# Kernel optimization log

Measured on AMD Instinct MI355X. Metric: run time of the kernel, lower is better.

The kernel has to match this reference:

```python
import jax, jax.numpy as jnp
import numpy as np

FEAS = 4096  # number of sparse features
K = 64       # FM latent factor dim
B = 4096     # batch size


def setup_inputs() -> dict:
    key = jax.random.key(0)
    k1, k2, k3, k4 = jax.random.split(key, 4)
    x = jax.random.normal(k1, (B, FEAS), dtype=jnp.float32)
    # torch.rand init for the cross factor tensor (feas, 1, k)
    cross = jax.random.uniform(k2, (FEAS, 1, K), dtype=jnp.float32)
    # nn.Linear(feas, 1): weight (1, feas), bias (1,)
    bound = 1.0 / np.sqrt(FEAS)
    linear_w = jax.random.uniform(k3, (1, FEAS), dtype=jnp.float32, minval=-bound, maxval=bound)
    linear_b = jax.random.uniform(k4, (1,), dtype=jnp.float32, minval=-bound, maxval=bound)
    return {"x": x, "cross": cross, "linear_w": linear_w, "linear_b": linear_b}


def reference(x, cross, linear_w, linear_b):
    # linear part: [B, feas] @ [feas, 1] + bias -> [B, 1]
    linear = x @ linear_w.T + linear_b

    # Cross term of the original: G[i, j] = V_i . V_j (Gram matrix of factor
    # vectors), summed over the upper triangle INCLUDING the diagonal.
    # sum_{i<=j} V_i.V_j = 0.5 * (sum_{i,j} V_i.V_j + sum_i ||V_i||^2)
    #                    = 0.5 * (||sum_i V_i||^2 + sum_i ||V_i||^2)
    # This avoids materializing the (feas, feas) matrix while computing the
    # exact same scalar.
    V = cross[:, 0, :]                      # (feas, k)
    col_sum = jnp.sum(V, axis=0)            # (k,)
    total = jnp.dot(col_sum, col_sum)       # sum over all (i, j) pairs
    diag = jnp.sum(V * V)                   # sum over i == j
    cross_sum = 0.5 * (total + diag)        # scalar, triu incl. diagonal

    # Note: the cross term is input-independent in the original module
    # (it never multiplies by the input); we reproduce that faithfully.
    return jax.nn.sigmoid(linear + cross_sum)
```

## Files before the change

### kernel.cpp

```cpp
#include <hip/hip_runtime.h>
#include <math.h>

#define FEAS 4096
#define K 64
#define BATCH 4096
#define NBLK 64

typedef float floatx4 __attribute__((ext_vector_type(4)));


__global__ __launch_bounds__(256) void cross_partial_kernel(
    const float* __restrict__ cross, float* __restrict__ ws) {
    const int j  = threadIdx.x & 63;
    const int rl = threadIdx.x >> 6;
    const int row0 = blockIdx.x * 64;

    float s = 0.f, q = 0.f;
#pragma unroll
    for (int i = 0; i < 16; ++i) {
        const float v = cross[(size_t)(row0 + rl * 16 + i) * K + j];
        s += v;
        q += v * v;
    }

    __shared__ float ls[256];
    __shared__ float lq[256];
    ls[threadIdx.x] = s;
    lq[threadIdx.x] = q;
    __syncthreads();

    if (threadIdx.x < 64) {
        const float cs = ls[j] + ls[j + 64] + ls[j + 128] + ls[j + 192];
        ws[blockIdx.x * 65 + j] = cs;

        float cq = lq[j] + lq[j + 64] + lq[j + 128] + lq[j + 192];
#pragma unroll
        for (int off = 32; off; off >>= 1) cq += __shfl_down(cq, off, 64);
        if (j == 0) ws[blockIdx.x * 65 + 64] = cq;
    }
}

__global__ __launch_bounds__(256) void gemv_sigmoid_kernel(
    const float* __restrict__ x, const float* __restrict__ w,
    const float* __restrict__ bias, const float* __restrict__ ws,
    float* __restrict__ out) {
    const int row = blockIdx.x;
    const int tid = threadIdx.x;

    __shared__ float s_cross;
    if (tid < 64) {
        float cs = 0.f;
#pragma unroll 8
        for (int b = 0; b < 64; ++b) cs += ws[b * 65 + tid];
        float val = cs * cs + ws[tid * 65 + 64];
#pragma unroll
        for (int off = 32; off; off >>= 1) val += __shfl_down(val, off, 64);
        if (tid == 0) s_cross = 0.5f * val;
    }

    const floatx4* __restrict__ xr = (const floatx4*)(x + (size_t)row * FEAS);
    const floatx4* __restrict__ wv = (const floatx4*)w;
    float acc = 0.f;
#pragma unroll
    for (int i = 0; i < 4; ++i) {
        const int idx = tid + i * 256;
        const floatx4 a = __builtin_nontemporal_load(&xr[idx]);
        const floatx4 b = wv[idx];
        acc += a.x * b.x + a.y * b.y + a.z * b.z + a.w * b.w;
    }

#pragma unroll
    for (int off = 32; off; off >>= 1) acc += __shfl_down(acc, off, 64);
    __shared__ float partial[4];
    if ((tid & 63) == 0) partial[tid >> 6] = acc;
    __syncthreads();

    if (tid == 0) {
        const float y = partial[0] + partial[1] + partial[2] + partial[3]
                        + bias[0] + s_cross;
        out[row] = 1.0f / (1.0f + expf(-y));
    }
}

extern "C" void kernel_launch(void* const* d_in, const int* in_sizes, int n_in,
                              void* d_out, int out_size, void* d_ws, size_t ws_size,
                              hipStream_t stream) {
    const float* x     = (const float*)d_in[0];
    const float* cross = (const float*)d_in[1];
    const float* w     = (const float*)d_in[2];
    const float* b     = (const float*)d_in[3];
    float* out = (float*)d_out;
    float* ws  = (float*)d_ws;

    cross_partial_kernel<<<NBLK, 256, 0, stream>>>(cross, ws);
    gemv_sigmoid_kernel<<<BATCH, 256, 0, stream>>>(x, w, b, ws, out);
}
```

Baseline: 107.4 us.

## Finalize cross-term reduction once via last-block atomic instead of per GEMV block

The first kernel now counts finished blocks with an atomic, and the last block to arrive sums all partial column sums and squares into a single scalar in workspace. Each GEMV block then reads that one value, where before all 4096 blocks redid the 64x65 reduction. The x loads also drop the nontemporal hint. A hipMemsetAsync is added every launch to reset the counter, which costs an extra stream operation.

```diff
diff --git a/kernel.cpp b/kernel.cpp
--- a/kernel.cpp
+++ b/kernel.cpp
@@ -8,8 +8,10 @@
 
 typedef float floatx4 __attribute__((ext_vector_type(4)));
 
+#define FINAL_IDX 4160
+#define CTR_IDX   4161
 
-__global__ __launch_bounds__(256) void cross_partial_kernel(
+__global__ __launch_bounds__(256) void cross_reduce_kernel(
     const float* __restrict__ cross, float* __restrict__ ws) {
     const int j  = threadIdx.x & 63;
     const int rl = threadIdx.x >> 6;
@@ -29,6 +31,7 @@
     lq[threadIdx.x] = q;
     __syncthreads();
 
+    __shared__ bool amLast;
     if (threadIdx.x < 64) {
         const float cs = ls[j] + ls[j + 64] + ls[j + 128] + ls[j + 192];
         ws[blockIdx.x * 65 + j] = cs;
@@ -36,7 +39,24 @@
         float cq = lq[j] + lq[j + 64] + lq[j + 128] + lq[j + 192];
 #pragma unroll
         for (int off = 32; off; off >>= 1) cq += __shfl_down(cq, off, 64);
-        if (j == 0) ws[blockIdx.x * 65 + 64] = cq;
+        if (j == 0) {
+            ws[blockIdx.x * 65 + 64] = cq;
+            __threadfence();
+            unsigned old = atomicAdd((unsigned*)&ws[CTR_IDX], 1u);
+            amLast = (old == NBLK - 1);
+        }
+    }
+    __syncthreads();
+
+    if (amLast && threadIdx.x < 64) {
+        __threadfence();
+        float csum = 0.f;
+#pragma unroll 8
+        for (int b = 0; b < NBLK; ++b) csum += ws[b * 65 + threadIdx.x];
+        float val = csum * csum + ws[threadIdx.x * 65 + 64];
+#pragma unroll
+        for (int off = 32; off; off >>= 1) val += __shfl_down(val, off, 64);
+        if (threadIdx.x == 0) ws[FINAL_IDX] = 0.5f * val;
     }
 }
 
@@ -47,16 +67,8 @@
     const int row = blockIdx.x;
     const int tid = threadIdx.x;
 
-    __shared__ float s_cross;
-    if (tid < 64) {
-        float cs = 0.f;
-#pragma unroll 8
-        for (int b = 0; b < 64; ++b) cs += ws[b * 65 + tid];
-        float val = cs * cs + ws[tid * 65 + 64];
-#pragma unroll
-        for (int off = 32; off; off >>= 1) val += __shfl_down(val, off, 64);
-        if (tid == 0) s_cross = 0.5f * val;
-    }
+    const float cross_sum = ws[FINAL_IDX];
+    const float b0 = bias[0];
 
     const floatx4* __restrict__ xr = (const floatx4*)(x + (size_t)row * FEAS);
     const floatx4* __restrict__ wv = (const floatx4*)w;
@@ -64,7 +76,7 @@
 #pragma unroll
     for (int i = 0; i < 4; ++i) {
         const int idx = tid + i * 256;
-        const floatx4 a = __builtin_nontemporal_load(&xr[idx]);
+        const floatx4 a = xr[idx];
         const floatx4 b = wv[idx];
         acc += a.x * b.x + a.y * b.y + a.z * b.z + a.w * b.w;
     }
@@ -77,7 +89,7 @@
 
     if (tid == 0) {
         const float y = partial[0] + partial[1] + partial[2] + partial[3]
-                        + bias[0] + s_cross;
+                        + b0 + cross_sum;
         out[row] = 1.0f / (1.0f + expf(-y));
     }
 }
@@ -92,6 +104,8 @@
     float* out = (float*)d_out;
     float* ws  = (float*)d_ws;
 
-    cross_partial_kernel<<<NBLK, 256, 0, stream>>>(cross, ws);
+    hipMemsetAsync(ws + CTR_IDX, 0, sizeof(unsigned), stream);
+
+    cross_reduce_kernel<<<NBLK, 256, 0, stream>>>(cross, ws);
     gemv_sigmoid_kernel<<<BATCH, 256, 0, stream>>>(x, w, b, ws, out);
 }
```

Result: faster. 101.7 us (-5.3%).
